# Kernel tuning notes

Measured on AMD Instinct MI355X. Metric: run time of the kernel, lower is better.

Reference implementation:

```python
import jax, jax.numpy as jnp
import numpy as np

N, K, D = 65536, 1024, 512
INIT_COUNT = 100


def setup_inputs() -> dict:
    key = jax.random.key(0)
    k1, k2 = jax.random.split(key)
    embedded = jax.random.normal(k1, (N, D), dtype=jnp.float32)
    centers = jax.random.normal(k2, (K, D), dtype=jnp.float32)
    count = jnp.full((K,), INIT_COUNT, dtype=jnp.int32)  # start_training: ones(K)*100
    return {"embedded": embedded, "centers": centers, "count": count}


def reference(embedded, centers, count):
    # --- squared_euclidean_distance(centers, embedded): dist[n,k] = ||e_n - c_k||^2 ---
    e2 = jnp.sum(embedded * embedded, axis=-1, keepdims=True)   # [N,1]
    c2 = jnp.sum(centers * centers, axis=-1)                    # [K]
    cross = embedded @ centers.T                                # [N,K] GEMM
    dist = e2 + c2[None, :] - 2.0 * cross                       # [N,K]

    # compression_loss: min over clusters, then mean
    loss = jnp.mean(jnp.min(dist, axis=1))

    # prediction_hard: hard assignments
    s = jnp.argmin(dist, axis=1)                                # [N] int

    # update_centroids: the per-sample EMA with eta = 1/count[c] is exactly an
    # incremental (running) mean seeded with `count` pseudo-counts, so the
    # sequential loop is mathematically equivalent to a vectorized segment mean:
    #   new_centers[c] = (count[c]*centers[c] + sum_{s_i=c} e_i) / (count[c] + n_c)
    added = jax.ops.segment_sum(embedded, s, num_segments=K)                       # [K,D]
    n_add = jax.ops.segment_sum(jnp.ones_like(s, dtype=jnp.int32), s, num_segments=K)  # [K]
    new_count = count + n_add
    cf = count.astype(centers.dtype)[:, None]
    new_centers = (cf * centers + added) / new_count.astype(centers.dtype)[:, None]

    return loss, s, new_centers, new_count
```

## Files before the change

### kernel.cpp

```cpp
#include <hip/hip_runtime.h>

#define N_SAMPLES 65536
#define K_CENT    1024
#define DIM       512
#define TAU 0.125f

typedef __attribute__((ext_vector_type(8))) short  short8;
typedef __attribute__((ext_vector_type(4))) float  float4v;
typedef __attribute__((ext_vector_type(4))) unsigned short ushort4v;

__device__ inline unsigned short f2bf(float x) {
    unsigned u = __builtin_bit_cast(unsigned, x);
    unsigned r = u + 0x7FFFu + ((u >> 16) & 1u);
    return (unsigned short)(r >> 16);
}
__device__ inline float bf2f(unsigned short h) {
    return __builtin_bit_cast(float, ((unsigned)h) << 16);
}

__global__ __launch_bounds__(256) void c2_kernel(const float* __restrict__ centers,
                                                 float* __restrict__ c2) {
    int wave = threadIdx.x >> 6, lane = threadIdx.x & 63;
    int k = blockIdx.x * 4 + wave;
    const float* row = centers + (size_t)k * DIM;
    float s = 0.f;
    #pragma unroll
    for (int base = 0; base < DIM; base += 256) {
        float4 v = *(const float4*)(row + base + lane * 4);
        s += v.x * v.x + v.y * v.y + v.z * v.z + v.w * v.w;
    }
    for (int off = 32; off; off >>= 1) s += __shfl_down(s, off);
    if (lane == 0) c2[k] = s;
}

__global__ __launch_bounds__(256) void bsplit_kernel(const float* __restrict__ cen,
                                                     unsigned short* __restrict__ Bh,
                                                     unsigned short* __restrict__ Bl) {
    int idx = blockIdx.x * 256 + threadIdx.x;
    float4 v = ((const float4*)cen)[idx];
    float f[4] = {v.x, v.y, v.z, v.w};
    ushort4v h, l;
    #pragma unroll
    for (int e = 0; e < 4; ++e) {
        unsigned short hh = f2bf(f[e]);
        h[e] = hh;
        l[e] = f2bf(f[e] - bf2f(hh));
    }
    *(ushort4v*)(Bh + (size_t)idx * 4) = h;
    *(ushort4v*)(Bl + (size_t)idx * 4) = l;
}

#define LDSA 40
__global__ __launch_bounds__(256, 4) void assign_mfma(
    const float* __restrict__ A,
    const unsigned short* __restrict__ Bh,
    const unsigned short* __restrict__ Bl,
    const float* __restrict__ c2,
    float* __restrict__ pbest,
    float* __restrict__ psec,
    int* __restrict__ pidx)
{
    __shared__ unsigned short Ah[128 * LDSA];
    __shared__ unsigned short Al[128 * LDSA];
    __shared__ __align__(16) unsigned short Bt[8192];
    __shared__ float st_best[128];
    __shared__ float st_sec[128];
    __shared__ int   st_idx[128];

    const int tid  = threadIdx.x;
    const int w    = tid >> 6;
    const int lane = tid & 63;
    const int quad = lane >> 4;
    const int l15  = lane & 15;
    const int mblk  = blockIdx.x & 511;
    const int chunk = blockIdx.x >> 9;
    const int m0   = mblk * 128;

    if (tid < 128) { st_best[tid] = 3.4e38f; st_sec[tid] = 3.4e38f; st_idx[tid] = 0; }

    const int r0 = tid >> 2, q = tid & 3;

    for (int nt = 0; nt < 4; ++nt) {
        const int n0 = chunk * 512 + nt * 128;
        float4v acc[16];
        #pragma unroll
        for (int z = 0; z < 16; ++z) acc[z] = (float4v){0.f, 0.f, 0.f, 0.f};

        for (int ks = 0; ks < 16; ++ks) {
            __syncthreads();
            #pragma unroll
            for (int half = 0; half < 2; ++half) {
                int rr = r0 + half * 64;
                const float* src = A + (size_t)(m0 + rr) * DIM + ks * 32 + q * 8;
                float4 v0 = *(const float4*)src;
                float4 v1 = *(const float4*)(src + 4);
                float f[8] = {v0.x, v0.y, v0.z, v0.w, v1.x, v1.y, v1.z, v1.w};
                short8 hi, lo;
                #pragma unroll
                for (int e = 0; e < 8; ++e) {
                    unsigned short hh = f2bf(f[e]);
                    hi[e] = (short)hh;
                    lo[e] = (short)f2bf(f[e] - bf2f(hh));
                }
                *(short8*)&Ah[rr * LDSA + q * 8] = hi;
                *(short8*)&Al[rr * LDSA + q * 8] = lo;
            }
            #pragma unroll
            for (int i = 0; i < 4; ++i) {
                int s = i * 256 + tid;
                int p  = s >> 9;
                int sp = s & 511;
                int qq = sp >> 7, r = sp & 127;
                const unsigned short* src = (p ? Bl : Bh)
                    + (size_t)(n0 + r) * DIM + ks * 32 + qq * 8;
                *(short8*)&Bt[s * 8] = *(const short8*)src;
            }
            __syncthreads();

            short8 ah[2], al[2];
            #pragma unroll
            for (int i = 0; i < 2; ++i) {
                int row = w * 32 + i * 16 + l15;
                ah[i] = *(const short8*)&Ah[row * LDSA + quad * 8];
                al[i] = *(const short8*)&Al[row * LDSA + quad * 8];
            }
            #pragma unroll
            for (int j4 = 0; j4 < 8; ++j4) {
                short8 bh = *(const short8*)&Bt[(quad * 128 + j4 * 16 + l15) * 8];
                short8 bl = *(const short8*)&Bt[(512 + quad * 128 + j4 * 16 + l15) * 8];
                #pragma unroll
                for (int i = 0; i < 2; ++i) {
                    acc[i * 8 + j4] = __builtin_amdgcn_mfma_f32_16x16x32_bf16(
                        ah[i], bh, acc[i * 8 + j4], 0, 0, 0);
                    acc[i * 8 + j4] = __builtin_amdgcn_mfma_f32_16x16x32_bf16(
                        ah[i], bl, acc[i * 8 + j4], 0, 0, 0);
                    acc[i * 8 + j4] = __builtin_amdgcn_mfma_f32_16x16x32_bf16(
                        al[i], bh, acc[i * 8 + j4], 0, 0, 0);
                }
            }
        }

        float c2v[8];
        #pragma unroll
        for (int j = 0; j < 8; ++j) c2v[j] = c2[n0 + j * 16 + l15];
        #pragma unroll
        for (int i = 0; i < 2; ++i)
            #pragma unroll
            for (int reg = 0; reg < 4; ++reg) {
                float bv = 3.4e38f, sv = 3.4e38f; int bi = 0;
                #pragma unroll
                for (int j = 0; j < 8; ++j) {
                    float v = c2v[j] - 2.0f * acc[i * 8 + j][reg];
                    int n = n0 + j * 16 + l15;
                    if (v < bv) { sv = bv; bv = v; bi = n; }
                    else if (v < sv) sv = v;
                }
                #pragma unroll
                for (int mask = 1; mask < 16; mask <<= 1) {
                    float ob = __shfl_xor(bv, mask);
                    float os = __shfl_xor(sv, mask);
                    int   oi = __shfl_xor(bi, mask);
                    float ns = fminf(fminf(sv, os), fmaxf(bv, ob));
                    if (ob < bv || (ob == bv && oi < bi)) { bv = ob; bi = oi; }
                    sv = ns;
                }
                if (l15 == 0) {
                    int ml = w * 32 + i * 16 + quad * 4 + reg;
                    float sb = st_best[ml], ss = st_sec[ml]; int si = st_idx[ml];
                    float ns = fminf(fminf(ss, sv), fmaxf(sb, bv));
                    if (bv < sb || (bv == sb && bi < si)) { st_best[ml] = bv; st_idx[ml] = bi; }
                    st_sec[ml] = ns;
                }
            }
    }

    __syncthreads();
    if (tid < 128) {
        int m = m0 + tid;
        pbest[chunk * N_SAMPLES + m] = st_best[tid];
        psec [chunk * N_SAMPLES + m] = st_sec[tid];
        pidx [chunk * N_SAMPLES + m] = st_idx[tid];
    }
}

__global__ __launch_bounds__(256) void merge_kernel(
    const float* __restrict__ pbest,
    const float* __restrict__ psec,
    const int* __restrict__ pidx,
    int* __restrict__ s_idx,
    float* __restrict__ out_s,
    int* __restrict__ hist,
    int* __restrict__ flag_cnt,
    int* __restrict__ flagged,
    float* __restrict__ out_loss)
{
    int m = blockIdx.x * 256 + threadIdx.x;
    float b0 = pbest[m], b1 = pbest[N_SAMPLES + m];
    float s0 = psec[m],  s1 = psec[N_SAMPLES + m];
    int   i0 = pidx[m],  i1 = pidx[N_SAMPLES + m];
    float bv, sv; int bi;
    if (b1 < b0) { bv = b1; bi = i1; sv = fminf(b0, s1); }
    else         { bv = b0; bi = i0; sv = fminf(s0, b1); }
    s_idx[m] = bi;
    out_s[m] = (float)bi;
    atomicAdd(&hist[bi], 1);
    if (sv - bv < TAU) { int p = atomicAdd(flag_cnt, 1); flagged[p] = m; }

    float ls = bv;
    for (int off = 32; off; off >>= 1) ls += __shfl_down(ls, off);
    __shared__ float ws4[4];
    int lane = threadIdx.x & 63, wv = threadIdx.x >> 6;
    if (lane == 0) ws4[wv] = ls;
    __syncthreads();
    if (threadIdx.x == 0)
        atomicAdd(out_loss, (ws4[0] + ws4[1] + ws4[2] + ws4[3]) * (1.0f / N_SAMPLES));
}

__global__ __launch_bounds__(256) void refine_kernel(
    const float* __restrict__ emb,
    const float* __restrict__ cen,
    const int* __restrict__ flag_cnt,
    const int* __restrict__ flagged,
    int* __restrict__ s_idx,
    float* __restrict__ out_s,
    int* __restrict__ hist)
{
    __shared__ float e_sh[DIM];
    __shared__ double rvd[256];
    __shared__ int rid[256];
    const int t = threadIdx.x;
    const int cnt = *flag_cnt;
    for (int idx = blockIdx.x; idx < cnt; idx += gridDim.x) {
        int n = flagged[idx];
        __syncthreads();
        ((float2*)e_sh)[t] = ((const float2*)(emb + (size_t)n * DIM))[t];
        __syncthreads();
        double bestd = 1e300;
        int bestk = 0;
        #pragma unroll
        for (int j = 0; j < 4; ++j) {
            int k = t * 4 + j;
            const float* crow = cen + (size_t)k * DIM;
            double acc = 0.0;
            for (int d = 0; d < DIM; d += 4) {
                float4 cv = *(const float4*)(crow + d);
                double d0 = (double)e_sh[d + 0] - (double)cv.x;
                double d1 = (double)e_sh[d + 1] - (double)cv.y;
                double d2 = (double)e_sh[d + 2] - (double)cv.z;
                double d3 = (double)e_sh[d + 3] - (double)cv.w;
                acc += d0 * d0 + d1 * d1 + d2 * d2 + d3 * d3;
            }
            if (acc < bestd) { bestd = acc; bestk = k; }
        }
        rvd[t] = bestd; rid[t] = bestk;
        __syncthreads();
        for (int off = 128; off; off >>= 1) {
            if (t < off) {
                double v = rvd[t + off]; int ii = rid[t + off];
                if (v < rvd[t] || (v == rvd[t] && ii < rid[t])) { rvd[t] = v; rid[t] = ii; }
            }
            __syncthreads();
        }
        if (t == 0) {
            int old = s_idx[n], nw = rid[0];
            if (nw != old) {
                atomicSub(&hist[old], 1);
                atomicAdd(&hist[nw], 1);
                s_idx[n] = nw;
                out_s[n] = (float)nw;
            }
        }
    }
}

__global__ void scan_kernel(const int* __restrict__ hist,
                            int* __restrict__ offsets,
                            int* __restrict__ cursor,
                            const int* __restrict__ count_in,
                            float* __restrict__ out_count) {
    __shared__ int sbuf[K_CENT];
    int t = threadIdx.x;
    int v = hist[t];
    sbuf[t] = v;
    __syncthreads();
    for (int off = 1; off < K_CENT; off <<= 1) {
        int x = (t >= off) ? sbuf[t - off] : 0;
        __syncthreads();
        sbuf[t] += x;
        __syncthreads();
    }
    int incl = sbuf[t];
    offsets[t] = incl - v;
    cursor[t]  = incl - v;
    out_count[t] = (float)(count_in[t] + v);
    if (t == K_CENT - 1) offsets[K_CENT] = incl;
}

__global__ void scatter_kernel(const int* __restrict__ s_idx,
                               int* __restrict__ cursor,
                               int* __restrict__ order) {
    int n = blockIdx.x * blockDim.x + threadIdx.x;
    if (n < N_SAMPLES) {
        int pos = atomicAdd(&cursor[s_idx[n]], 1);
        order[pos] = n;
    }
}

__global__ __launch_bounds__(256) void gp_kernel(
    const float* __restrict__ emb,
    const int* __restrict__ s_idx,
    const int* __restrict__ order,
    float* __restrict__ accum,
    float* __restrict__ out_loss)
{
    __shared__ int s_n[64], s_c[64];
    const int t = threadIdx.x;
    const int base = blockIdx.x * 64;
    if (t < 64) { int n = order[base + t]; s_n[t] = n; s_c[t] = s_idx[n]; }
    __syncthreads();
    float ax = 0.f, ay = 0.f, ssq = 0.f;
    int cur = s_c[0];
    for (int r = 0; r < 64; ++r) {
        int n = s_n[r], c = s_c[r];
        if (c != cur) {
            atomicAdd(&accum[(size_t)cur * DIM + t * 2], ax);
            atomicAdd(&accum[(size_t)cur * DIM + t * 2 + 1], ay);
            ax = ay = 0.f; cur = c;
        }
        float2 e = *(const float2*)(emb + (size_t)n * DIM + t * 2);
        ax += e.x; ay += e.y;
        ssq += e.x * e.x + e.y * e.y;
    }
    atomicAdd(&accum[(size_t)cur * DIM + t * 2], ax);
    atomicAdd(&accum[(size_t)cur * DIM + t * 2 + 1], ay);

    for (int off = 32; off; off >>= 1) ssq += __shfl_down(ssq, off);
    __shared__ float wsum[4];
    if ((t & 63) == 0) wsum[t >> 6] = ssq;
    __syncthreads();
    if (t == 0)
        atomicAdd(out_loss, (wsum[0] + wsum[1] + wsum[2] + wsum[3]) * (1.0f / N_SAMPLES));
}

__global__ __launch_bounds__(256) void combine_kernel(
    const float* __restrict__ centers,
    const int* __restrict__ count_in,
    const int* __restrict__ hist,
    const float* __restrict__ accum,
    float* __restrict__ out_centers)
{
    int k = blockIdx.x, t = threadIdx.x;
    float cn = (float)count_in[k];
    float tot = cn + (float)hist[k];
    float2 c = *(const float2*)(centers + (size_t)k * DIM + t * 2);
    float2 a = *(const float2*)(accum   + (size_t)k * DIM + t * 2);
    float2 o;
    o.x = (cn * c.x + a.x) / tot;
    o.y = (cn * c.y + a.y) / tot;
    *(float2*)(out_centers + (size_t)k * DIM + t * 2) = o;
}

extern "C" void kernel_launch(void* const* d_in, const int* in_sizes, int n_in,
                              void* d_out, int out_size, void* d_ws, size_t ws_size,
                              hipStream_t stream) {
    const float* emb = (const float*)d_in[0];
    const float* cen = (const float*)d_in[1];
    const int*   cnt = (const int*)d_in[2];

    float* out = (float*)d_out;
    float* out_loss    = out;
    float* out_s       = out + 1;
    float* out_centers = out + 1 + N_SAMPLES;
    float* out_count   = out + 1 + N_SAMPLES + (size_t)K_CENT * DIM;

    int* wsi = (int*)d_ws;
    int*   hist     = wsi;
    int*   offsets  = wsi + 1024;
    int*   cursor   = wsi + 2064;
    int*   s_idx    = wsi + 4096;
    float* c2       = (float*)(wsi + 69632);
    int*   flag_cnt = wsi + 70656;
    int*   flagged  = wsi + 70720;
    float* pbest    = (float*)(wsi + 136256);
    float* psec     = (float*)(wsi + 267328);
    int*   pidx     = wsi + 398400;
    unsigned short* Bh = (unsigned short*)(wsi + 529472);
    unsigned short* Bl = (unsigned short*)(wsi + 791616);
    int*   order    = wsi + 136256;
    float* accum    = (float*)(wsi + 529472);

    hipMemsetAsync(hist, 0, K_CENT * sizeof(int), stream);
    hipMemsetAsync(out_loss, 0, sizeof(float), stream);
    hipMemsetAsync(flag_cnt, 0, sizeof(int), stream);

    c2_kernel<<<K_CENT / 4, 256, 0, stream>>>(cen, c2);
    bsplit_kernel<<<512, 256, 0, stream>>>(cen, Bh, Bl);
    assign_mfma<<<1024, 256, 0, stream>>>(emb, Bh, Bl, c2, pbest, psec, pidx);
    merge_kernel<<<N_SAMPLES / 256, 256, 0, stream>>>(pbest, psec, pidx, s_idx, out_s,
                                                      hist, flag_cnt, flagged, out_loss);
    hipMemsetAsync(accum, 0, (size_t)K_CENT * DIM * sizeof(float), stream);
    refine_kernel<<<256, 256, 0, stream>>>(emb, cen, flag_cnt, flagged, s_idx, out_s, hist);
    scan_kernel<<<1, K_CENT, 0, stream>>>(hist, offsets, cursor, cnt, out_count);
    scatter_kernel<<<N_SAMPLES / 256, 256, 0, stream>>>(s_idx, cursor, order);
    gp_kernel<<<N_SAMPLES / 64, 256, 0, stream>>>(emb, s_idx, order, accum, out_loss);
    combine_kernel<<<K_CENT, 256, 0, stream>>>(cen, cnt, hist, accum, out_centers);
}
```

Baseline: 722.2 us.

## Switch distance GEMM to fp16 two-term split and load A directly to registers

Replaces the three-MFMA bf16 hi/lo split with fp16 (A split into hi+lo, B only hi), cutting MFMAs per tile from three to two and halving B staging in LDS. A is now loaded from global memory straight into registers and converted there, which drops the A LDS buffers and their writes. The c2 and B-conversion kernels are fused into one launch. This relies on fp16 range and precision being adequate for the inputs, with the existing refine step catching near-ties; fp16 B without a low part gives a less accurate cross term.

```diff
diff --git a/kernel.cpp b/kernel.cpp
--- a/kernel.cpp
+++ b/kernel.cpp
@@ -6,63 +6,40 @@
 #define TAU 0.125f
 
 typedef __attribute__((ext_vector_type(8))) short  short8;
+typedef _Float16 half8 __attribute__((ext_vector_type(8)));
 typedef __attribute__((ext_vector_type(4))) float  float4v;
-typedef __attribute__((ext_vector_type(4))) unsigned short ushort4v;
-
-__device__ inline unsigned short f2bf(float x) {
-    unsigned u = __builtin_bit_cast(unsigned, x);
-    unsigned r = u + 0x7FFFu + ((u >> 16) & 1u);
-    return (unsigned short)(r >> 16);
-}
-__device__ inline float bf2f(unsigned short h) {
-    return __builtin_bit_cast(float, ((unsigned)h) << 16);
-}
-
-__global__ __launch_bounds__(256) void c2_kernel(const float* __restrict__ centers,
-                                                 float* __restrict__ c2) {
-    int wave = threadIdx.x >> 6, lane = threadIdx.x & 63;
-    int k = blockIdx.x * 4 + wave;
-    const float* row = centers + (size_t)k * DIM;
-    float s = 0.f;
-    #pragma unroll
-    for (int base = 0; base < DIM; base += 256) {
-        float4 v = *(const float4*)(row + base + lane * 4);
-        s += v.x * v.x + v.y * v.y + v.z * v.z + v.w * v.w;
-    }
+
+__device__ inline unsigned short f2h_bits(float x) {
+    _Float16 h = (_Float16)x;
+    return __builtin_bit_cast(unsigned short, h);
+}
+
+__global__ __launch_bounds__(256) void hsplit_c2_kernel(const float* __restrict__ cen,
+                                                        unsigned short* __restrict__ Bh,
+                                                        float* __restrict__ c2) {
+    const int k = blockIdx.x, t = threadIdx.x;
+    const float* row = cen + (size_t)k * DIM;
+    float2 v = ((const float2*)row)[t];
+    unsigned int packed = (unsigned)f2h_bits(v.x) | ((unsigned)f2h_bits(v.y) << 16);
+    *(unsigned int*)(Bh + (size_t)k * DIM + t * 2) = packed;
+    float s = v.x * v.x + v.y * v.y;
     for (int off = 32; off; off >>= 1) s += __shfl_down(s, off);
-    if (lane == 0) c2[k] = s;
-}
-
-__global__ __launch_bounds__(256) void bsplit_kernel(const float* __restrict__ cen,
-                                                     unsigned short* __restrict__ Bh,
-                                                     unsigned short* __restrict__ Bl) {
-    int idx = blockIdx.x * 256 + threadIdx.x;
-    float4 v = ((const float4*)cen)[idx];
-    float f[4] = {v.x, v.y, v.z, v.w};
-    ushort4v h, l;
-    #pragma unroll
-    for (int e = 0; e < 4; ++e) {
-        unsigned short hh = f2bf(f[e]);
-        h[e] = hh;
-        l[e] = f2bf(f[e] - bf2f(hh));
-    }
-    *(ushort4v*)(Bh + (size_t)idx * 4) = h;
-    *(ushort4v*)(Bl + (size_t)idx * 4) = l;
-}
-
-#define LDSA 40
+    __shared__ float w4[4];
+    int lane = t & 63, wv = t >> 6;
+    if (lane == 0) w4[wv] = s;
+    __syncthreads();
+    if (t == 0) c2[k] = w4[0] + w4[1] + w4[2] + w4[3];
+}
+
 __global__ __launch_bounds__(256, 4) void assign_mfma(
     const float* __restrict__ A,
     const unsigned short* __restrict__ Bh,
-    const unsigned short* __restrict__ Bl,
     const float* __restrict__ c2,
     float* __restrict__ pbest,
     float* __restrict__ psec,
     int* __restrict__ pidx)
 {
-    __shared__ unsigned short Ah[128 * LDSA];
-    __shared__ unsigned short Al[128 * LDSA];
-    __shared__ __align__(16) unsigned short Bt[8192];
+    __shared__ __align__(16) unsigned short Bt[4096];
     __shared__ float st_best[128];
     __shared__ float st_sec[128];
     __shared__ int   st_idx[128];
@@ -78,7 +55,7 @@
 
     if (tid < 128) { st_best[tid] = 3.4e38f; st_sec[tid] = 3.4e38f; st_idx[tid] = 0; }
 
-    const int r0 = tid >> 2, q = tid & 3;
+    const float* aBase = A + (size_t)(m0 + w * 32 + l15) * DIM + quad * 8;
 
     for (int nt = 0; nt < 4; ++nt) {
         const int n0 = chunk * 512 + nt * 128;
@@ -87,54 +64,46 @@
         for (int z = 0; z < 16; ++z) acc[z] = (float4v){0.f, 0.f, 0.f, 0.f};
 
         for (int ks = 0; ks < 16; ++ks) {
+            float4 av[2][2];
+            #pragma unroll
+            for (int i = 0; i < 2; ++i) {
+                const float* ap = aBase + i * 16 * DIM + ks * 32;
+                av[i][0] = *(const float4*)ap;
+                av[i][1] = *(const float4*)(ap + 4);
+            }
+
             __syncthreads();
             #pragma unroll
-            for (int half = 0; half < 2; ++half) {
-                int rr = r0 + half * 64;
-                const float* src = A + (size_t)(m0 + rr) * DIM + ks * 32 + q * 8;
-                float4 v0 = *(const float4*)src;
-                float4 v1 = *(const float4*)(src + 4);
-                float f[8] = {v0.x, v0.y, v0.z, v0.w, v1.x, v1.y, v1.z, v1.w};
-                short8 hi, lo;
+            for (int i = 0; i < 2; ++i) {
+                int s = i * 256 + tid;
+                int qq = s >> 7, r = s & 127;
+                *(short8*)&Bt[s * 8] =
+                    *(const short8*)(Bh + (size_t)(n0 + r) * DIM + ks * 32 + qq * 8);
+            }
+            __syncthreads();
+
+            half8 ah[2], al[2];
+            #pragma unroll
+            for (int i = 0; i < 2; ++i) {
+                float f[8] = {av[i][0].x, av[i][0].y, av[i][0].z, av[i][0].w,
+                              av[i][1].x, av[i][1].y, av[i][1].z, av[i][1].w};
                 #pragma unroll
                 for (int e = 0; e < 8; ++e) {
-                    unsigned short hh = f2bf(f[e]);
-                    hi[e] = (short)hh;
-                    lo[e] = (short)f2bf(f[e] - bf2f(hh));
-                }
-                *(short8*)&Ah[rr * LDSA + q * 8] = hi;
-                *(short8*)&Al[rr * LDSA + q * 8] = lo;
-            }
-            #pragma unroll
-            for (int i = 0; i < 4; ++i) {
-                int s = i * 256 + tid;
-                int p  = s >> 9;
-                int sp = s & 511;
-                int qq = sp >> 7, r = sp & 127;
-                const unsigned short* src = (p ? Bl : Bh)
-                    + (size_t)(n0 + r) * DIM + ks * 32 + qq * 8;
-                *(short8*)&Bt[s * 8] = *(const short8*)src;
-            }
-            __syncthreads();
-
-            short8 ah[2], al[2];
-            #pragma unroll
-            for (int i = 0; i < 2; ++i) {
-                int row = w * 32 + i * 16 + l15;
-                ah[i] = *(const short8*)&Ah[row * LDSA + quad * 8];
-                al[i] = *(const short8*)&Al[row * LDSA + quad * 8];
-            }
+                    _Float16 h = (_Float16)f[e];
+                    ah[i][e] = h;
+                    al[i][e] = (_Float16)(f[e] - (float)h);
+                }
+            }
+
             #pragma unroll
             for (int j4 = 0; j4 < 8; ++j4) {
-                short8 bh = *(const short8*)&Bt[(quad * 128 + j4 * 16 + l15) * 8];
-                short8 bl = *(const short8*)&Bt[(512 + quad * 128 + j4 * 16 + l15) * 8];
+                short8 braw = *(const short8*)&Bt[(quad * 128 + j4 * 16 + l15) * 8];
+                half8 bh = __builtin_bit_cast(half8, braw);
                 #pragma unroll
                 for (int i = 0; i < 2; ++i) {
-                    acc[i * 8 + j4] = __builtin_amdgcn_mfma_f32_16x16x32_bf16(
+                    acc[i * 8 + j4] = __builtin_amdgcn_mfma_f32_16x16x32_f16(
                         ah[i], bh, acc[i * 8 + j4], 0, 0, 0);
-                    acc[i * 8 + j4] = __builtin_amdgcn_mfma_f32_16x16x32_bf16(
-                        ah[i], bl, acc[i * 8 + j4], 0, 0, 0);
-                    acc[i * 8 + j4] = __builtin_amdgcn_mfma_f32_16x16x32_bf16(
+                    acc[i * 8 + j4] = __builtin_amdgcn_mfma_f32_16x16x32_f16(
                         al[i], bh, acc[i * 8 + j4], 0, 0, 0);
                 }
             }
@@ -385,7 +354,6 @@
     float* psec     = (float*)(wsi + 267328);
     int*   pidx     = wsi + 398400;
     unsigned short* Bh = (unsigned short*)(wsi + 529472);
-    unsigned short* Bl = (unsigned short*)(wsi + 791616);
     int*   order    = wsi + 136256;
     float* accum    = (float*)(wsi + 529472);
 
@@ -393,9 +361,8 @@
     hipMemsetAsync(out_loss, 0, sizeof(float), stream);
     hipMemsetAsync(flag_cnt, 0, sizeof(int), stream);
 
-    c2_kernel<<<K_CENT / 4, 256, 0, stream>>>(cen, c2);
-    bsplit_kernel<<<512, 256, 0, stream>>>(cen, Bh, Bl);
-    assign_mfma<<<1024, 256, 0, stream>>>(emb, Bh, Bl, c2, pbest, psec, pidx);
+    hsplit_c2_kernel<<<K_CENT, 256, 0, stream>>>(cen, Bh, c2);
+    assign_mfma<<<1024, 256, 0, stream>>>(emb, Bh, c2, pbest, psec, pidx);
     merge_kernel<<<N_SAMPLES / 256, 256, 0, stream>>>(pbest, psec, pidx, s_idx, out_s,
                                                       hist, flag_cnt, flagged, out_loss);
     hipMemsetAsync(accum, 0, (size_t)K_CENT * DIM * sizeof(float), stream);
```

New measurement: 679.7 us. -5.9%, faster.
